# Optimization experiments

Measured on AMD Instinct MI355X. Metric: run time of the kernel, lower is better.

## Reference

```python
import jax, jax.numpy as jnp
import numpy as np

EPS = 1e-6
INV_T = 100.0
STEPS = 7  # eval_steps


def setup_inputs() -> dict:
    key = jax.random.key(0)
    k1, k2 = jax.random.split(key)
    B, C, H, W, R = 8, 512, 128, 128, 64
    x = jax.random.uniform(k1, (B, C, H, W), dtype=jnp.float32)
    bases = jax.random.uniform(k2, (B, C, R), dtype=jnp.float32)
    # _build_bases: F.normalize(bases, dim=1) -> L2 normalize over D
    bases = bases / jnp.maximum(jnp.linalg.norm(bases, axis=1, keepdims=True), 1e-12)
    return {"x": x, "bases": bases}


def _nmf(xf, bases):
    # xf: [B, D, N], bases: [B, D, R]
    # coef init: softmax(inv_t * x^T @ bases) over R
    coef = jax.nn.softmax(INV_T * jnp.einsum('bdn,bdr->bnr', xf, bases), axis=-1)

    def step(carry, _):
        bases, coef = carry
        # multiplicative update for coef: coef * (x^T B) / (coef (B^T B))
        num = jnp.einsum('bdn,bdr->bnr', xf, bases)          # [B,N,R]
        den = coef @ (jnp.swapaxes(bases, 1, 2) @ bases)      # [B,N,R]
        coef = coef * num / (den + EPS)
        # multiplicative update for bases: B * (x coef) / (B (coef^T coef))
        num = jnp.einsum('bdn,bnr->bdr', xf, coef)            # [B,D,R]
        den = bases @ (jnp.swapaxes(coef, 1, 2) @ coef)       # [B,D,R]
        bases = bases * num / (den + EPS)
        return (bases, coef), None

    (bases, coef), _ = jax.lax.scan(step, (bases, coef), None, length=STEPS)
    # compute_coef: one final coef update
    num = jnp.einsum('bdn,bdr->bnr', xf, bases)
    den = coef @ (jnp.swapaxes(bases, 1, 2) @ bases)
    coef = coef * num / (den + EPS)
    return bases, coef


def reference(x, bases):
    B, C, H, W = x.shape
    N = H * W
    xf = x.reshape(B, C, N)  # S=1, D=C
    bases, coef = _nmf(xf, bases)
    out = jnp.einsum('bdr,bnr->bdn', bases, coef)  # bases @ coef^T
    return out.reshape(B, C, H, W)
```

## Files before the change

kernel.cpp:

```cpp
#include <hip/hip_runtime.h>
#include <cstdint>
#include <cstddef>

namespace {

constexpr int B_ = 8;
constexpr int D_ = 512;
constexpr int N_ = 16384;
constexpr int R_ = 64;
constexpr float EPS_ = 1e-6f;
constexpr float INVT_ = 100.0f;

typedef __attribute__((ext_vector_type(4))) float f32x4;
typedef __attribute__((ext_vector_type(8))) short s16x8;
typedef __attribute__((ext_vector_type(4))) short s16x4;

#define MFMA16(A, Bv, C) __builtin_amdgcn_mfma_f32_16x16x32_bf16(A, Bv, C, 0, 0, 0)

#define VMW(n) asm volatile("s_waitcnt vmcnt(" #n ")" ::: "memory")
#define LGKM0 asm volatile("s_waitcnt lgkmcnt(0)" ::: "memory")
#define SCHEDB __builtin_amdgcn_sched_barrier(0)
#define BARRIER do { SCHEDB; __builtin_amdgcn_s_barrier(); SCHEDB; } while (0)

typedef __attribute__((address_space(3))) unsigned int lds_u32_t;
typedef const __attribute__((address_space(1))) unsigned int glb_u32_t;

__device__ __forceinline__ void gl2lds16(const void* g, void* l) {
    __builtin_amdgcn_global_load_lds((glb_u32_t*)g, (lds_u32_t*)l, 16, 0, 0);
}

__device__ __forceinline__ unsigned short f2bf(float x) {
    unsigned int u = __float_as_uint(x);
    return (unsigned short)((u + 0x7fffu + ((u >> 16) & 1u)) >> 16);
}
__device__ __forceinline__ float bf2f(unsigned short u) {
    return __uint_as_float(((unsigned int)u) << 16);
}
__device__ __forceinline__ s16x8 ld8(const unsigned short* p) {
    return *reinterpret_cast<const s16x8*>(p);
}

__device__ __forceinline__ void stage16(const unsigned short* __restrict__ rowbase,
        size_t rstride_elems, unsigned short* __restrict__ buf, int w, int lane) {
#pragma unroll
    for (int i = 0; i < 4; ++i) {
        int r = w * 4 + i;
        const char* src = reinterpret_cast<const char*>(rowbase + (size_t)r * rstride_elems)
                        + ((lane << 4) ^ ((r & 7) << 4));
        gl2lds16(src, reinterpret_cast<char*>(buf) + r * 1024);
    }
}
__device__ __forceinline__ s16x8 read_t16(const unsigned short* buf, int row, int ks, int h4) {
    return *reinterpret_cast<const s16x8*>(reinterpret_cast<const char*>(buf)
        + row * 1024 + ((ks * 64 + h4 * 16) ^ ((row & 7) << 4)));
}
__device__ __forceinline__ void stage_c16(const unsigned short* __restrict__ cnr_n0,
        unsigned short* __restrict__ buf, int w, int lane) {
    int h = w & 1;
    int row = h * 8 + (lane >> 3);
    const char* src = reinterpret_cast<const char*>(cnr_n0 + (size_t)row * R_)
                    + ((((lane & 7) ^ (row & 7))) << 4);
    gl2lds16(src, reinterpret_cast<char*>(buf) + h * 1024);
}
__device__ __forceinline__ s16x8 read_c16(const unsigned short* buf, int row, int ks, int h4) {
    return *reinterpret_cast<const s16x8*>(reinterpret_cast<const char*>(buf)
        + row * 128 + ((ks * 64 + h4 * 16) ^ ((row & 7) << 4)));
}
__device__ __forceinline__ float read_c_scalar(const unsigned short* buf, int row, int r) {
    return bf2f(*reinterpret_cast<const unsigned short*>(
        reinterpret_cast<const char*>(buf) + row * 128 + ((r * 2) ^ ((row & 7) << 4))));
}

__global__ __launch_bounds__(256) void k_convert(const float* __restrict__ X,
        unsigned short* __restrict__ Xhi, unsigned short* __restrict__ XThi,
        unsigned short* __restrict__ XTlo, int have_lo) {
    __shared__ f32x4 lds4[64 * 16];
    int id = blockIdx.x;
    int nblk = id & 255, dblk = (id >> 8) & 7, b = id >> 11;
    int t = threadIdx.x;
    int d = t >> 2, c0 = (t & 3) * 16;
    const float* Xb = X + ((size_t)b * D_ + dblk * 64) * N_ + (size_t)nblk * 64;
    f32x4 v[4];
#pragma unroll
    for (int i = 0; i < 4; ++i)
        v[i] = *reinterpret_cast<const f32x4*>(Xb + (size_t)d * N_ + c0 + 4 * i);
    {
        int swz = (d ^ (d >> 3)) & 7;
#pragma unroll
        for (int i = 0; i < 4; ++i)
            lds4[d * 16 + ((((t & 3) << 2) + i) ^ swz)] = v[i];
    }
    {
        unsigned short* dst = Xhi + ((size_t)b * D_ + dblk * 64 + d) * N_
                            + (size_t)nblk * 64 + c0;
        s16x8 h0, h1;
#pragma unroll
        for (int k = 0; k < 8; ++k) {
            h0[k] = (short)f2bf(v[k >> 2][k & 3]);
            h1[k] = (short)f2bf(v[2 + (k >> 2)][k & 3]);
        }
        *reinterpret_cast<s16x8*>(dst) = h0;
        *reinterpret_cast<s16x8*>(dst + 8) = h1;
    }
    __syncthreads();
    {
        int n = t >> 2;
        const float* L = reinterpret_cast<const float*>(lds4);
        s16x8 h0, h1, l0, l1;
#pragma unroll
        for (int k = 0; k < 16; ++k) {
            int r = c0 + k;
            int sz = (r ^ (r >> 3)) & 7;
            float a = L[r * 64 + ((((n >> 2) ^ sz) << 2) | (n & 3))];
            unsigned short ha = f2bf(a);
            unsigned short la = f2bf(a - bf2f(ha));
            if (k < 8) { h0[k] = (short)ha; l0[k] = (short)la; }
            else       { h1[k - 8] = (short)ha; l1[k - 8] = (short)la; }
        }
        size_t off = ((size_t)b * N_ + nblk * 64 + n) * D_ + dblk * 64 + c0;
        *reinterpret_cast<s16x8*>(XThi + off) = h0;
        *reinterpret_cast<s16x8*>(XThi + off + 8) = h1;
        if (have_lo) {
            *reinterpret_cast<s16x8*>(XTlo + off) = l0;
            *reinterpret_cast<s16x8*>(XTlo + off + 8) = l1;
        }
    }
}

__global__ __launch_bounds__(256) void k_ginit(const float* __restrict__ Bin,
        float* __restrict__ bases, unsigned short* __restrict__ BThi,
        unsigned short* __restrict__ BTlo) {
    __shared__ float lds[64][65];
    int id = blockIdx.x, dblk = id & 7, b = id >> 3;
    int t = threadIdx.x, tn = t & 63, tq = t >> 6;
    const float* Bb = Bin + ((size_t)b * D_ + dblk * 64) * R_;
    float* bb = bases + ((size_t)b * D_ + dblk * 64) * R_;
#pragma unroll
    for (int i = 0; i < 16; ++i) {
        int d = i * 4 + tq;
        float v = Bb[d * R_ + tn];
        lds[d][tn] = v;
        bb[d * R_ + tn] = v;
    }
    __syncthreads();
#pragma unroll
    for (int i = 0; i < 16; ++i) {
        int r = i * 4 + tq;
        float v = lds[tn][r];
        unsigned short hi = f2bf(v);
        size_t off = ((size_t)b * R_ + r) * D_ + dblk * 64 + tn;
        BThi[off] = hi;
        BTlo[off] = f2bf(v - bf2f(hi));
    }
}

__global__ __launch_bounds__(256) void k_gram(const unsigned short* __restrict__ BT,
        unsigned short* __restrict__ G) {
    int b = blockIdx.x;
    int t = threadIdx.x, lane = t & 63, w = t >> 6;
    int m16 = lane & 15, h4 = lane >> 4;
    const unsigned short* BTb = BT + (size_t)b * R_ * D_;
    f32x4 acc[4];
#pragma unroll
    for (int j = 0; j < 4; ++j) acc[j] = (f32x4){0.f, 0.f, 0.f, 0.f};
#pragma unroll
    for (int k0 = 0; k0 < D_; k0 += 32) {
        int kg = k0 + (h4 << 3);
        s16x8 frag[4];
#pragma unroll
        for (int j = 0; j < 4; ++j)
            frag[j] = ld8(BTb + (size_t)(j * 16 + m16) * D_ + kg);
        s16x8 fw = ld8(BTb + (size_t)(w * 16 + m16) * D_ + kg);
#pragma unroll
        for (int j = 0; j < 4; ++j) acc[j] = MFMA16(fw, frag[j], acc[j]);
    }
    unsigned short* Gb = G + (size_t)b * R_ * R_;
#pragma unroll
    for (int j = 0; j < 4; ++j)
#pragma unroll
        for (int q = 0; q < 4; ++q) {
            int r1 = 16 * w + (h4 << 2) + q;
            Gb[r1 * R_ + 16 * j + m16] = f2bf(acc[j][q]);
        }
}

template <int LO>
__global__ __launch_bounds__(256, 2) void k_init(const unsigned short* __restrict__ XThi,
        const unsigned short* __restrict__ XTlo, const unsigned short* __restrict__ BThi,
        const unsigned short* __restrict__ BTlo, const unsigned short* __restrict__ G,
        unsigned short* __restrict__ CTb, unsigned short* __restrict__ Cnr) {
    __shared__ __align__(16) unsigned short xhbuf[2][16 * 512];
    __shared__ __align__(16) unsigned short xlbuf[LO ? 2 : 1][16 * 512];
    __shared__ __align__(16) unsigned short ldsc[16 * 64];
    __shared__ float red[2][4][16];
    int id = blockIdx.x, blk = id & 63, b = id >> 6;
    int t = threadIdx.x, lane = t & 63, w = t >> 6;
    int m16 = lane & 15, h4 = lane >> 4;
    const unsigned short* XTb = XThi + (size_t)b * N_ * D_;
    const unsigned short* XLb = XTlo + (size_t)b * N_ * D_;
    const unsigned short* BThb = BThi + (size_t)b * R_ * D_;
    const unsigned short* BTlb = BTlo + (size_t)b * R_ * D_;
    const unsigned short* Gb = G + (size_t)b * R_ * R_;
    unsigned short* CTbb = CTb + (size_t)b * R_ * N_;
    unsigned short* Cnrb = Cnr + (size_t)b * N_ * R_;
    s16x8 abh[16], abl[16], g[2];
#pragma unroll
    for (int ks = 0; ks < 16; ++ks) {
        size_t off = (size_t)(w * 16 + m16) * D_ + ks * 32 + h4 * 8;
        abh[ks] = ld8(BThb + off);
        abl[ks] = ld8(BTlb + off);
    }
#pragma unroll
    for (int ks = 0; ks < 2; ++ks)
        g[ks] = ld8(Gb + (size_t)(w * 16 + m16) * R_ + ks * 32 + h4 * 8);
    SCHEDB;
    stage16(XTb + (size_t)(blk * 16 + 0) * 16 * D_, D_, xhbuf[0], w, lane);
    if (LO) stage16(XLb + (size_t)(blk * 16 + 0) * 16 * D_, D_, xlbuf[0], w, lane);
    stage16(XTb + (size_t)(blk * 16 + 1) * 16 * D_, D_, xhbuf[1], w, lane);
    if (LO) stage16(XLb + (size_t)(blk * 16 + 1) * 16 * D_, D_, xlbuf[1], w, lane);
    SCHEDB;

    int swz = (m16 & 7) << 4;
    char* crow = reinterpret_cast<char*>(ldsc) + m16 * 128;

    for (int tt = 0; tt < 16; ++tt) {
        int cur = tt & 1;
        int n0 = (blk * 16 + tt) * 16;
        if (LO) {
            if (tt == 0) VMW(8);
            else if (tt == 15) VMW(5);
            else VMW(13);
        } else {
            if (tt == 0) VMW(4);
            else if (tt == 15) VMW(5);
            else VMW(9);
        }
        BARRIER;
        const unsigned short* xh = xhbuf[cur];
        const unsigned short* xl = xlbuf[LO ? cur : 0];
        f32x4 acc = (f32x4){0.f, 0.f, 0.f, 0.f};
#pragma unroll
        for (int ks = 0; ks < 16; ++ks) {
            s16x8 bh = read_t16(xh, m16, ks, h4);
            acc = MFMA16(abh[ks], bh, acc);
            acc = MFMA16(abl[ks], bh, acc);
            if (LO) {
                s16x8 bl = read_t16(xl, m16, ks, h4);
                acc = MFMA16(abh[ks], bl, acc);
            }
        }
        float mx = fmaxf(fmaxf(acc[0], acc[1]), fmaxf(acc[2], acc[3]));
        mx = fmaxf(mx, __shfl_xor(mx, 16));
        mx = fmaxf(mx, __shfl_xor(mx, 32));
        if (lane < 16) red[0][w][m16] = mx;
        LGKM0; BARRIER;
        mx = fmaxf(fmaxf(red[0][0][m16], red[0][1][m16]),
                   fmaxf(red[0][2][m16], red[0][3][m16]));
        float p[4], ss = 0.f;
#pragma unroll
        for (int q = 0; q < 4; ++q) {
            p[q] = __expf(INVT_ * (acc[q] - mx));
            ss += p[q];
        }
        ss += __shfl_xor(ss, 16);
        ss += __shfl_xor(ss, 32);
        if (lane < 16) red[1][w][m16] = ss;
        LGKM0; BARRIER;
        ss = red[1][0][m16] + red[1][1][m16] + red[1][2][m16] + red[1][3][m16];
        float inv = 1.f / ss;
#pragma unroll
        for (int q = 0; q < 4; ++q) {
            int r = w * 16 + h4 * 4 + q;
            *reinterpret_cast<unsigned short*>(crow + ((r * 2) ^ swz)) = f2bf(p[q] * inv);
        }
        LGKM0; BARRIER;
        f32x4 dacc = (f32x4){0.f, 0.f, 0.f, 0.f};
#pragma unroll
        for (int ks = 0; ks < 2; ++ks) {
            s16x8 bf = *reinterpret_cast<const s16x8*>(crow + ((ks * 64 + h4 * 16) ^ swz));
            dacc = MFMA16(g[ks], bf, dacc);
        }
        s16x4 cn;
        float c1v[4];
#pragma unroll
        for (int q = 0; q < 4; ++q) {
            c1v[q] = p[q] * inv * acc[q] / (dacc[q] + EPS_);
            cn[q] = (short)f2bf(c1v[q]);
        }
        LGKM0; BARRIER;
        SCHEDB;
#pragma unroll
        for (int q = 0; q < 4; ++q)
            CTbb[(size_t)(w * 16 + h4 * 4 + q) * N_ + n0 + m16] = f2bf(c1v[q]);
        *reinterpret_cast<s16x4*>(Cnrb + (size_t)(n0 + m16) * R_ + w * 16 + h4 * 4) = cn;
        SCHEDB;
        if (tt + 2 < 16) {
            stage16(XTb + (size_t)(blk * 16 + tt + 2) * 16 * D_, D_, xhbuf[cur], w, lane);
            if (LO) stage16(XLb + (size_t)(blk * 16 + tt + 2) * 16 * D_, D_, xlbuf[cur], w, lane);
        }
        SCHEDB;
    }
}

__global__ __launch_bounds__(256, 4) void k_cu(const unsigned short* __restrict__ XThi,
        const unsigned short* __restrict__ BThi, const unsigned short* __restrict__ G,
        unsigned short* __restrict__ CTb, unsigned short* __restrict__ Cnr) {
    __shared__ __align__(16) unsigned short xbuf[2][16 * 512];
    __shared__ __align__(16) unsigned short cbuf[2][16 * 64];
    int id = blockIdx.x, blk = id & 127, b = id >> 7;
    int t = threadIdx.x, lane = t & 63, w = t >> 6;
    int m16 = lane & 15, h4 = lane >> 4;
    const unsigned short* XTb = XThi + (size_t)b * N_ * D_;
    const unsigned short* BTb = BThi + (size_t)b * R_ * D_;
    const unsigned short* Gb = G + (size_t)b * R_ * R_;
    unsigned short* CTbb = CTb + (size_t)b * R_ * N_;
    unsigned short* Cnrb = Cnr + (size_t)b * N_ * R_;
    s16x8 abt[16], g[2];
#pragma unroll
    for (int ks = 0; ks < 16; ++ks)
        abt[ks] = ld8(BTb + (size_t)(w * 16 + m16) * D_ + ks * 32 + h4 * 8);
#pragma unroll
    for (int ks = 0; ks < 2; ++ks)
        g[ks] = ld8(Gb + (size_t)(w * 16 + m16) * R_ + ks * 32 + h4 * 8);
    SCHEDB;
    stage16(XTb + (size_t)(blk * 8 + 0) * 16 * D_, D_, xbuf[0], w, lane);
    stage_c16(Cnrb + (size_t)(blk * 8 + 0) * 16 * R_, cbuf[0], w, lane);
    stage16(XTb + (size_t)(blk * 8 + 1) * 16 * D_, D_, xbuf[1], w, lane);
    stage_c16(Cnrb + (size_t)(blk * 8 + 1) * 16 * R_, cbuf[1], w, lane);
    SCHEDB;

    for (int tt = 0; tt < 8; ++tt) {
        int cur = tt & 1;
        int n0 = (blk * 8 + tt) * 16;
        if (tt == 0) VMW(5);
        else if (tt == 7) VMW(5);
        else VMW(10);
        BARRIER;
        const unsigned short* xb = xbuf[cur];
        const unsigned short* cb = cbuf[cur];
        f32x4 acc = (f32x4){0.f, 0.f, 0.f, 0.f};
#pragma unroll
        for (int ks = 0; ks < 16; ++ks)
            acc = MFMA16(abt[ks], read_t16(xb, m16, ks, h4), acc);
        f32x4 dacc = (f32x4){0.f, 0.f, 0.f, 0.f};
#pragma unroll
        for (int ks = 0; ks < 2; ++ks)
            dacc = MFMA16(g[ks], read_c16(cb, m16, ks, h4), dacc);
        s16x4 cn;
        float c1v[4];
#pragma unroll
        for (int q = 0; q < 4; ++q) {
            int r = w * 16 + h4 * 4 + q;
            float cold = read_c_scalar(cb, m16, r);
            c1v[q] = cold * acc[q] / (dacc[q] + EPS_);
            cn[q] = (short)f2bf(c1v[q]);
        }
        LGKM0; BARRIER;
        SCHEDB;
#pragma unroll
        for (int q = 0; q < 4; ++q)
            CTbb[(size_t)(w * 16 + h4 * 4 + q) * N_ + n0 + m16] = f2bf(c1v[q]);
        *reinterpret_cast<s16x4*>(Cnrb + (size_t)(n0 + m16) * R_ + w * 16 + h4 * 4) = cn;
        SCHEDB;
        if (tt + 2 < 8) {
            stage16(XTb + (size_t)(blk * 8 + tt + 2) * 16 * D_, D_, xbuf[cur], w, lane);
            stage_c16(Cnrb + (size_t)(blk * 8 + tt + 2) * 16 * R_, cbuf[cur], w, lane);
        }
        SCHEDB;
    }
}

__global__ __launch_bounds__(256, 4) void k_bu1t(const unsigned short* __restrict__ Xhi,
        const unsigned short* __restrict__ CTb, unsigned short* __restrict__ wsN2,
        float* __restrict__ wsH) {
    __shared__ __align__(16) unsigned short xbuf[2][16 * 512];
    int id = blockIdx.x;
    int b = id >> 7, c = (id >> 2) & 31, dg = id & 3;
    int t = threadIdx.x, lane = t & 63, w = t >> 6;
    int m16 = lane & 15, h4 = lane >> 4;
    const unsigned short* Xb = Xhi + (size_t)b * D_ * N_ + c * 512;
    const unsigned short* Cbc = CTb + (size_t)b * R_ * N_ + c * 512;
    s16x8 act[16];
#pragma unroll
    for (int ks = 0; ks < 16; ++ks)
        act[ks] = ld8(Cbc + (size_t)(w * 16 + m16) * N_ + ks * 32 + h4 * 8);
    f32x4 hacc = (f32x4){0.f, 0.f, 0.f, 0.f};
    {
        const unsigned short* Hrow = Cbc + (size_t)(dg * 16 + m16) * N_;
#pragma unroll
        for (int gg = 0; gg < 4; ++gg) {
            SCHEDB;
            s16x8 hb[4];
#pragma unroll
            for (int j = 0; j < 4; ++j)
                hb[j] = ld8(Hrow + (gg * 4 + j) * 32 + h4 * 8);
#pragma unroll
            for (int j = 0; j < 4; ++j)
                hacc = MFMA16(act[gg * 4 + j], hb[j], hacc);
        }
    }
    SCHEDB;
    stage16(Xb + (size_t)(dg * 128 + 0) * N_, N_, xbuf[0], w, lane);
    stage16(Xb + (size_t)(dg * 128 + 16) * N_, N_, xbuf[1], w, lane);
    SCHEDB;
    unsigned short* n2 = wsN2 + (size_t)(b * 32 + c) * R_ * D_;
    for (int tt = 0; tt < 8; ++tt) {
        int cur = tt & 1;
        int d0 = dg * 128 + tt * 16;
        if (tt == 0) VMW(4);
        else if (tt == 7) VMW(4);
        else VMW(8);
        BARRIER;
        const unsigned short* xb = xbuf[cur];
        f32x4 acc = (f32x4){0.f, 0.f, 0.f, 0.f};
#pragma unroll
        for (int ks = 0; ks < 16; ++ks)
            acc = MFMA16(act[ks], read_t16(xb, m16, ks, h4), acc);
        LGKM0; BARRIER;
        SCHEDB;
        if (tt + 2 < 8)
            stage16(Xb + (size_t)(dg * 128 + (tt + 2) * 16) * N_, N_, xbuf[cur], w, lane);
        SCHEDB;
#pragma unroll
        for (int q = 0; q < 4; ++q)
            n2[(size_t)(w * 16 + h4 * 4 + q) * D_ + d0 + m16] = f2bf(acc[q]);
        SCHEDB;
    }
    float* Hp = wsH + (size_t)(b * 32 + c) * 4096;
#pragma unroll
    for (int q = 0; q < 4; ++q)
        Hp[(w * 16 + h4 * 4 + q) * R_ + dg * 16 + m16] = hacc[q];
}

__global__ __launch_bounds__(256) void k_hred(const float* __restrict__ wsH,
        float* __restrict__ Hf) {
    int id = blockIdx.x, q = id & 3, b = id >> 2;
    int t = threadIdx.x;
    int i = q * 1024 + t * 4;
    f32x4 s = (f32x4){0.f, 0.f, 0.f, 0.f};
    for (int c = 0; c < 32; ++c)
        s += *reinterpret_cast<const f32x4*>(wsH + ((size_t)b * 32 + c) * 4096 + i);
    *reinterpret_cast<f32x4*>(Hf + (size_t)b * 4096 + i) = s;
}

__global__ __launch_bounds__(256) void k_bu2(const unsigned short* __restrict__ wsN2,
        const float* __restrict__ Hf, float* __restrict__ bases,
        unsigned short* __restrict__ BThi, unsigned short* __restrict__ Bdr) {
    __shared__ float ldsH[64][64];
    __shared__ float ldsb[16][65];
    __shared__ float ldsn[16][65];
    int id = blockIdx.x, dblk = id & 31, b = id >> 5;
    int t = threadIdx.x;
    int d0 = dblk * 16;
    const float* Hb = Hf + (size_t)b * 4096;
#pragma unroll
    for (int i = 0; i < 4; ++i) {
        f32x4 v = *reinterpret_cast<const f32x4*>(Hb + i * 1024 + t * 4);
        *reinterpret_cast<f32x4*>(&ldsH[0][0] + i * 1024 + t * 4) = v;
    }
    {
        int d = t >> 4, p0 = (t & 15) * 4;
        f32x4 v = *reinterpret_cast<const f32x4*>(bases + ((size_t)b * D_ + d0 + d) * R_ + p0);
#pragma unroll
        for (int k = 0; k < 4; ++k) ldsb[d][p0 + k] = v[k];
    }
    __syncthreads();
#pragma unroll
    for (int j = 0; j < 4; ++j) {
        int i = t + 256 * j;
        int r = i >> 4, d = i & 15;
        float n2 = 0.f;
        for (int c = 0; c < 32; ++c)
            n2 += bf2f(wsN2[(((size_t)b * 32 + c) * R_ + r) * D_ + d0 + d]);
        float den = 0.f;
#pragma unroll 8
        for (int p = 0; p < 64; ++p) den += ldsb[d][p] * ldsH[p][r];
        ldsn[d][r] = ldsb[d][r] * n2 / (den + EPS_);
    }
    __syncthreads();
    {
        int d = t >> 4, r0 = (t & 15) * 4;
        f32x4 v;
        s16x4 hv;
#pragma unroll
        for (int k = 0; k < 4; ++k) {
            v[k] = ldsn[d][r0 + k];
            hv[k] = (short)f2bf(v[k]);
        }
        *reinterpret_cast<f32x4*>(bases + ((size_t)b * D_ + d0 + d) * R_ + r0) = v;
        *reinterpret_cast<s16x4*>((unsigned short*)Bdr + ((size_t)b * D_ + d0 + d) * R_ + r0) = hv;
    }
    {
        int r = t >> 2, dd = (t & 3) * 4;
        s16x4 hv;
#pragma unroll
        for (int k = 0; k < 4; ++k) hv[k] = (short)f2bf(ldsn[dd + k][r]);
        *reinterpret_cast<s16x4*>(BThi + ((size_t)b * R_ + r) * D_ + d0 + dd) = hv;
    }
}

__global__ __launch_bounds__(256, 2) void k_out(const unsigned short* __restrict__ Bdr,
        const unsigned short* __restrict__ Cnr, float* __restrict__ Out) {
    __shared__ float ldso[4][64 * 68 + 8];
    int id = blockIdx.x, nblk = id & 63, dblk = (id >> 6) & 7, b = id >> 9;
    int t = threadIdx.x, lane = t & 63, w = t >> 6;
    int m16 = lane & 15, h4 = lane >> 4;
    const unsigned short* Bb = Bdr + (size_t)b * D_ * R_;
    const unsigned short* Cb = Cnr + (size_t)b * N_ * R_;
    int d0 = dblk * 64, n0 = nblk * 256 + w * 64;
    f32x4 acc[4][4];
#pragma unroll
    for (int i = 0; i < 4; ++i)
#pragma unroll
        for (int j = 0; j < 4; ++j) acc[i][j] = (f32x4){0.f, 0.f, 0.f, 0.f};
#pragma unroll
    for (int k0 = 0; k0 < 64; k0 += 32) {
        int kg = k0 + (h4 << 3);
        s16x8 afrag[4], bfrag[4];
#pragma unroll
        for (int i = 0; i < 4; ++i)
            afrag[i] = ld8(Bb + (size_t)(d0 + i * 16 + m16) * R_ + kg);
#pragma unroll
        for (int j = 0; j < 4; ++j)
            bfrag[j] = ld8(Cb + (size_t)(n0 + j * 16 + m16) * R_ + kg);
#pragma unroll
        for (int i = 0; i < 4; ++i)
#pragma unroll
            for (int j = 0; j < 4; ++j)
                acc[i][j] = MFMA16(afrag[i], bfrag[j], acc[i][j]);
    }
#pragma unroll
    for (int i = 0; i < 4; ++i)
#pragma unroll
        for (int j = 0; j < 4; ++j)
#pragma unroll
            for (int q = 0; q < 4; ++q)
                ldso[w][(i * 16 + h4 * 4 + q) * 68 + j * 16 + m16] = acc[i][j][q];
    __syncthreads();
    float* Ob = Out + (size_t)b * D_ * N_ + (size_t)d0 * N_ + nblk * 256;
    int quad = lane >> 4, cc = (lane & 15) * 4;
#pragma unroll
    for (int i = 0; i < 16; ++i) {
        int d = w * 16 + i;
        f32x4 v = *reinterpret_cast<const f32x4*>(&ldso[quad][d * 68 + cc]);
        *reinterpret_cast<f32x4*>(Ob + (size_t)d * N_ + quad * 64 + cc) = v;
    }
}

}

extern "C" void kernel_launch(void* const* d_in, const int* in_sizes, int n_in,
                              void* d_out, int out_size, void* d_ws, size_t ws_size,
                              hipStream_t stream) {
    const float* X = (const float*)d_in[0];
    const float* Bin = (const float*)d_in[1];
    float* Out = (float*)d_out;
    char* ws = (char*)d_ws;

    const size_t o_Xhi  = 0;
    const size_t o_XThi = o_Xhi  + (size_t)B_ * D_ * N_ * 2;
    const size_t o_CTb  = o_XThi + (size_t)B_ * N_ * D_ * 2;
    const size_t o_Cnr  = o_CTb  + (size_t)B_ * R_ * N_ * 2;
    const size_t o_bas  = o_Cnr  + (size_t)B_ * N_ * R_ * 2;
    const size_t o_BThi = o_bas  + (size_t)B_ * D_ * R_ * 4;
    const size_t o_BTlo = o_BThi + (size_t)B_ * R_ * D_ * 2;
    const size_t o_Bdr  = o_BTlo + (size_t)B_ * R_ * D_ * 2;
    const size_t o_G    = o_Bdr  + (size_t)B_ * D_ * R_ * 2;
    const size_t o_H    = o_G    + (size_t)B_ * R_ * R_ * 2;
    const size_t o_Hf   = o_H    + (size_t)B_ * 32 * R_ * R_ * 4;
    const size_t o_N2   = o_Hf   + (size_t)B_ * R_ * R_ * 4;
    const size_t BASE   = o_N2   + (size_t)B_ * 32 * R_ * D_ * 2;
    const size_t o_XTlo = BASE;
    const size_t FULL   = o_XTlo + (size_t)B_ * N_ * D_ * 2;

    if (ws_size < BASE) return;
    int have_lo = ws_size >= FULL ? 1 : 0;

    unsigned short* Xhi  = (unsigned short*)(ws + o_Xhi);
    unsigned short* XThi = (unsigned short*)(ws + o_XThi);
    unsigned short* XTlo = (unsigned short*)(ws + (have_lo ? o_XTlo : o_XThi));
    unsigned short* CTb  = (unsigned short*)(ws + o_CTb);
    unsigned short* Cnr  = (unsigned short*)(ws + o_Cnr);
    float*          bas  = (float*)(ws + o_bas);
    unsigned short* BThi = (unsigned short*)(ws + o_BThi);
    unsigned short* BTlo = (unsigned short*)(ws + o_BTlo);
    unsigned short* Bdr  = (unsigned short*)(ws + o_Bdr);
    unsigned short* G    = (unsigned short*)(ws + o_G);
    float*          H    = (float*)(ws + o_H);
    float*          Hf   = (float*)(ws + o_Hf);
    unsigned short* N2   = (unsigned short*)(ws + o_N2);

    k_convert<<<dim3(16384), dim3(256), 0, stream>>>(X, Xhi, XThi, XTlo, have_lo);
    k_ginit<<<dim3(64), dim3(256), 0, stream>>>(Bin, bas, BThi, BTlo);
    k_gram<<<dim3(8), dim3(256), 0, stream>>>(BThi, G);
    if (have_lo)
        k_init<1><<<dim3(512), dim3(256), 0, stream>>>(XThi, XTlo, BThi, BTlo, G, CTb, Cnr);
    else
        k_init<0><<<dim3(512), dim3(256), 0, stream>>>(XThi, XTlo, BThi, BTlo, G, CTb, Cnr);
    for (int s = 0; s < 7; ++s) {
        k_bu1t<<<dim3(1024), dim3(256), 0, stream>>>(Xhi, CTb, N2, H);
        k_hred<<<dim3(32), dim3(256), 0, stream>>>(H, Hf);
        k_bu2<<<dim3(256), dim3(256), 0, stream>>>(N2, Hf, bas, BThi, Bdr);
        k_gram<<<dim3(8), dim3(256), 0, stream>>>(BThi, G);
        k_cu<<<dim3(1024), dim3(256), 0, stream>>>(XThi, BThi, G, CTb, Cnr);
    }
    k_out<<<dim3(4096), dim3(256), 0, stream>>>(Bdr, Cnr, Out);
}
```

Before: 1.222 ms.

## Process batch in groups so per-group working set stays cache-resident across iterations

Adds a batch-offset parameter to the iterative kernels and runs all NMF iterations plus the output for a group of 4 batches before moving to the next group. The aim is to keep each group's bf16 copies of X and the coefficient buffers resident in the last-level cache across the 7 iterations, instead of streaming the whole batch from HBM every step. The cost is twice as many kernel launches, and each grid is half as large, which may underfill the GPU.

```diff
diff --git a/kernel.cpp b/kernel.cpp
--- a/kernel.cpp
+++ b/kernel.cpp
@@ -10,6 +10,7 @@
 constexpr int R_ = 64;
 constexpr float EPS_ = 1e-6f;
 constexpr float INVT_ = 100.0f;
+constexpr int GB_ = 4;
 
 typedef __attribute__((ext_vector_type(4))) float f32x4;
 typedef __attribute__((ext_vector_type(8))) short s16x8;
@@ -155,8 +156,8 @@
 }
 
 __global__ __launch_bounds__(256) void k_gram(const unsigned short* __restrict__ BT,
-        unsigned short* __restrict__ G) {
-    int b = blockIdx.x;
+        unsigned short* __restrict__ G, int b0) {
+    int b = b0 + blockIdx.x;
     int t = threadIdx.x, lane = t & 63, w = t >> 6;
     int m16 = lane & 15, h4 = lane >> 4;
     const unsigned short* BTb = BT + (size_t)b * R_ * D_;
@@ -304,10 +305,10 @@
 
 __global__ __launch_bounds__(256, 4) void k_cu(const unsigned short* __restrict__ XThi,
         const unsigned short* __restrict__ BThi, const unsigned short* __restrict__ G,
-        unsigned short* __restrict__ CTb, unsigned short* __restrict__ Cnr) {
+        unsigned short* __restrict__ CTb, unsigned short* __restrict__ Cnr, int b0) {
     __shared__ __align__(16) unsigned short xbuf[2][16 * 512];
     __shared__ __align__(16) unsigned short cbuf[2][16 * 64];
-    int id = blockIdx.x, blk = id & 127, b = id >> 7;
+    int id = blockIdx.x, blk = id & 127, b = b0 + (id >> 7);
     int t = threadIdx.x, lane = t & 63, w = t >> 6;
     int m16 = lane & 15, h4 = lane >> 4;
     const unsigned short* XTb = XThi + (size_t)b * N_ * D_;
@@ -372,10 +373,10 @@
 
 __global__ __launch_bounds__(256, 4) void k_bu1t(const unsigned short* __restrict__ Xhi,
         const unsigned short* __restrict__ CTb, unsigned short* __restrict__ wsN2,
-        float* __restrict__ wsH) {
+        float* __restrict__ wsH, int b0) {
     __shared__ __align__(16) unsigned short xbuf[2][16 * 512];
     int id = blockIdx.x;
-    int b = id >> 7, c = (id >> 2) & 31, dg = id & 3;
+    int b = b0 + (id >> 7), c = (id >> 2) & 31, dg = id & 3;
     int t = threadIdx.x, lane = t & 63, w = t >> 6;
     int m16 = lane & 15, h4 = lane >> 4;
     const unsigned short* Xb = Xhi + (size_t)b * D_ * N_ + c * 512;
@@ -433,8 +434,8 @@
 }
 
 __global__ __launch_bounds__(256) void k_hred(const float* __restrict__ wsH,
-        float* __restrict__ Hf) {
-    int id = blockIdx.x, q = id & 3, b = id >> 2;
+        float* __restrict__ Hf, int b0) {
+    int id = blockIdx.x, q = id & 3, b = b0 + (id >> 2);
     int t = threadIdx.x;
     int i = q * 1024 + t * 4;
     f32x4 s = (f32x4){0.f, 0.f, 0.f, 0.f};
@@ -445,11 +446,11 @@
 
 __global__ __launch_bounds__(256) void k_bu2(const unsigned short* __restrict__ wsN2,
         const float* __restrict__ Hf, float* __restrict__ bases,
-        unsigned short* __restrict__ BThi, unsigned short* __restrict__ Bdr) {
+        unsigned short* __restrict__ BThi, unsigned short* __restrict__ Bdr, int b0) {
     __shared__ float ldsH[64][64];
     __shared__ float ldsb[16][65];
     __shared__ float ldsn[16][65];
-    int id = blockIdx.x, dblk = id & 31, b = id >> 5;
+    int id = blockIdx.x, dblk = id & 31, b = b0 + (id >> 5);
     int t = threadIdx.x;
     int d0 = dblk * 16;
     const float* Hb = Hf + (size_t)b * 4096;
@@ -500,9 +501,9 @@
 }
 
 __global__ __launch_bounds__(256, 2) void k_out(const unsigned short* __restrict__ Bdr,
-        const unsigned short* __restrict__ Cnr, float* __restrict__ Out) {
+        const unsigned short* __restrict__ Cnr, float* __restrict__ Out, int b0) {
     __shared__ float ldso[4][64 * 68 + 8];
-    int id = blockIdx.x, nblk = id & 63, dblk = (id >> 6) & 7, b = id >> 9;
+    int id = blockIdx.x, nblk = id & 63, dblk = (id >> 6) & 7, b = b0 + (id >> 9);
     int t = threadIdx.x, lane = t & 63, w = t >> 6;
     int m16 = lane & 15, h4 = lane >> 4;
     const unsigned short* Bb = Bdr + (size_t)b * D_ * R_;
@@ -592,17 +593,20 @@
 
     k_convert<<<dim3(16384), dim3(256), 0, stream>>>(X, Xhi, XThi, XTlo, have_lo);
     k_ginit<<<dim3(64), dim3(256), 0, stream>>>(Bin, bas, BThi, BTlo);
-    k_gram<<<dim3(8), dim3(256), 0, stream>>>(BThi, G);
+    k_gram<<<dim3(B_), dim3(256), 0, stream>>>(BThi, G, 0);
     if (have_lo)
         k_init<1><<<dim3(512), dim3(256), 0, stream>>>(XThi, XTlo, BThi, BTlo, G, CTb, Cnr);
     else
         k_init<0><<<dim3(512), dim3(256), 0, stream>>>(XThi, XTlo, BThi, BTlo, G, CTb, Cnr);
-    for (int s = 0; s < 7; ++s) {
-        k_bu1t<<<dim3(1024), dim3(256), 0, stream>>>(Xhi, CTb, N2, H);
-        k_hred<<<dim3(32), dim3(256), 0, stream>>>(H, Hf);
-        k_bu2<<<dim3(256), dim3(256), 0, stream>>>(N2, Hf, bas, BThi, Bdr);
-        k_gram<<<dim3(8), dim3(256), 0, stream>>>(BThi, G);
-        k_cu<<<dim3(1024), dim3(256), 0, stream>>>(XThi, BThi, G, CTb, Cnr);
-    }
-    k_out<<<dim3(4096), dim3(256), 0, stream>>>(Bdr, Cnr, Out);
-}
+    for (int g = 0; g < B_ / GB_; ++g) {
+        int b0 = g * GB_;
+        for (int s = 0; s < 7; ++s) {
+            k_bu1t<<<dim3(GB_ * 128), dim3(256), 0, stream>>>(Xhi, CTb, N2, H, b0);
+            k_hred<<<dim3(GB_ * 4), dim3(256), 0, stream>>>(H, Hf, b0);
+            k_bu2<<<dim3(GB_ * 32), dim3(256), 0, stream>>>(N2, Hf, bas, BThi, Bdr, b0);
+            k_gram<<<dim3(GB_), dim3(256), 0, stream>>>(BThi, G, b0);
+            k_cu<<<dim3(GB_ * 128), dim3(256), 0, stream>>>(XThi, BThi, G, CTb, Cnr, b0);
+        }
+        k_out<<<dim3(GB_ * 512), dim3(256), 0, stream>>>(Bdr, Cnr, Out, b0);
+    }
+}
```

Result: slower. 1.356 ms (+10.9%).

## Fuse Gram computation into coef update and swizzle block IDs across XCDs

Applied to the files above, without the earlier changes.

Removes the separate k_gram launch inside the iteration loop by having each k_cu block recompute its 16 rows of the 64x64 bases Gram matrix with MFMAs. The result goes through LDS, reusing the second X staging buffer before it is filled. Block indices in k_init, k_cu, k_bu1t and k_out are also remapped so each of the 8 XCDs handles one batch, which should improve per-XCD L2 locality. In exchange, every k_cu block redoes the Gram work and reads more BThi data, adding some redundant compute and loads in place of a tiny serial kernel launch and its dependency gap.

```diff
diff --git a/kernel.cpp b/kernel.cpp
--- a/kernel.cpp
+++ b/kernel.cpp
@@ -193,7 +193,9 @@
     __shared__ __align__(16) unsigned short xlbuf[LO ? 2 : 1][16 * 512];
     __shared__ __align__(16) unsigned short ldsc[16 * 64];
     __shared__ float red[2][4][16];
-    int id = blockIdx.x, blk = id & 63, b = id >> 6;
+    int id0 = blockIdx.x;
+    int id = (id0 & 7) * 64 + (id0 >> 3);
+    int blk = id & 63, b = id >> 6;
     int t = threadIdx.x, lane = t & 63, w = t >> 6;
     int m16 = lane & 15, h4 = lane >> 4;
     const unsigned short* XTb = XThi + (size_t)b * N_ * D_;
@@ -303,28 +305,53 @@
 }
 
 __global__ __launch_bounds__(256, 4) void k_cu(const unsigned short* __restrict__ XThi,
-        const unsigned short* __restrict__ BThi, const unsigned short* __restrict__ G,
+        const unsigned short* __restrict__ BThi,
         unsigned short* __restrict__ CTb, unsigned short* __restrict__ Cnr) {
     __shared__ __align__(16) unsigned short xbuf[2][16 * 512];
     __shared__ __align__(16) unsigned short cbuf[2][16 * 64];
-    int id = blockIdx.x, blk = id & 127, b = id >> 7;
+    int id0 = blockIdx.x;
+    int id = (id0 & 7) * 128 + (id0 >> 3);
+    int blk = id & 127, b = id >> 7;
     int t = threadIdx.x, lane = t & 63, w = t >> 6;
     int m16 = lane & 15, h4 = lane >> 4;
     const unsigned short* XTb = XThi + (size_t)b * N_ * D_;
     const unsigned short* BTb = BThi + (size_t)b * R_ * D_;
-    const unsigned short* Gb = G + (size_t)b * R_ * R_;
     unsigned short* CTbb = CTb + (size_t)b * R_ * N_;
     unsigned short* Cnrb = Cnr + (size_t)b * N_ * R_;
-    s16x8 abt[16], g[2];
+    s16x8 abt[16];
 #pragma unroll
     for (int ks = 0; ks < 16; ++ks)
         abt[ks] = ld8(BTb + (size_t)(w * 16 + m16) * D_ + ks * 32 + h4 * 8);
-#pragma unroll
-    for (int ks = 0; ks < 2; ++ks)
-        g[ks] = ld8(Gb + (size_t)(w * 16 + m16) * R_ + ks * 32 + h4 * 8);
     SCHEDB;
     stage16(XTb + (size_t)(blk * 8 + 0) * 16 * D_, D_, xbuf[0], w, lane);
     stage_c16(Cnrb + (size_t)(blk * 8 + 0) * 16 * R_, cbuf[0], w, lane);
+    SCHEDB;
+    f32x4 gacc[4];
+#pragma unroll
+    for (int j = 0; j < 4; ++j) gacc[j] = (f32x4){0.f, 0.f, 0.f, 0.f};
+#pragma unroll
+    for (int ks = 0; ks < 16; ++ks) {
+        s16x8 fr[4];
+#pragma unroll
+        for (int j = 0; j < 4; ++j)
+            fr[j] = ld8(BTb + (size_t)(j * 16 + m16) * D_ + ks * 32 + h4 * 8);
+#pragma unroll
+        for (int j = 0; j < 4; ++j) gacc[j] = MFMA16(abt[ks], fr[j], gacc[j]);
+    }
+    unsigned short* gs = xbuf[1] + w * 1024;
+#pragma unroll
+    for (int j = 0; j < 4; ++j)
+#pragma unroll
+        for (int q = 0; q < 4; ++q)
+            gs[(h4 * 4 + q) * 64 + j * 16 + m16] = f2bf(gacc[j][q]);
+    LGKM0;
+    s16x8 g[2];
+#pragma unroll
+    for (int ks = 0; ks < 2; ++ks)
+        g[ks] = ld8(gs + m16 * 64 + ks * 32 + h4 * 8);
+    LGKM0;
+    BARRIER;
+    SCHEDB;
     stage16(XTb + (size_t)(blk * 8 + 1) * 16 * D_, D_, xbuf[1], w, lane);
     stage_c16(Cnrb + (size_t)(blk * 8 + 1) * 16 * R_, cbuf[1], w, lane);
     SCHEDB;
@@ -374,7 +401,8 @@
         const unsigned short* __restrict__ CTb, unsigned short* __restrict__ wsN2,
         float* __restrict__ wsH) {
     __shared__ __align__(16) unsigned short xbuf[2][16 * 512];
-    int id = blockIdx.x;
+    int id0 = blockIdx.x;
+    int id = (id0 & 7) * 128 + (id0 >> 3);
     int b = id >> 7, c = (id >> 2) & 31, dg = id & 3;
     int t = threadIdx.x, lane = t & 63, w = t >> 6;
     int m16 = lane & 15, h4 = lane >> 4;
@@ -502,7 +530,9 @@
 __global__ __launch_bounds__(256, 2) void k_out(const unsigned short* __restrict__ Bdr,
         const unsigned short* __restrict__ Cnr, float* __restrict__ Out) {
     __shared__ float ldso[4][64 * 68 + 8];
-    int id = blockIdx.x, nblk = id & 63, dblk = (id >> 6) & 7, b = id >> 9;
+    int id0 = blockIdx.x;
+    int id = (id0 & 7) * 512 + (id0 >> 3);
+    int nblk = id & 63, dblk = (id >> 6) & 7, b = id >> 9;
     int t = threadIdx.x, lane = t & 63, w = t >> 6;
     int m16 = lane & 15, h4 = lane >> 4;
     const unsigned short* Bb = Bdr + (size_t)b * D_ * R_;
@@ -601,8 +631,7 @@
         k_bu1t<<<dim3(1024), dim3(256), 0, stream>>>(Xhi, CTb, N2, H);
         k_hred<<<dim3(32), dim3(256), 0, stream>>>(H, Hf);
         k_bu2<<<dim3(256), dim3(256), 0, stream>>>(N2, Hf, bas, BThi, Bdr);
-        k_gram<<<dim3(8), dim3(256), 0, stream>>>(BThi, G);
-        k_cu<<<dim3(1024), dim3(256), 0, stream>>>(XThi, BThi, G, CTb, Cnr);
+        k_cu<<<dim3(1024), dim3(256), 0, stream>>>(XThi, BThi, CTb, Cnr);
     }
     k_out<<<dim3(4096), dim3(256), 0, stream>>>(Bdr, Cnr, Out);
 }
```

Measured after the change: 1.454 ms. +18.9%, slower.
